# Performance work log

Measured on AMD Instinct MI355X. Metric: run time of the kernel, lower is better.

## Reference

```python
import jax, jax.numpy as jnp
import numpy as np

# Model dims (see init_kwargs)
B, N, N_IN, D = 16, 8192, 4096, 8
DT = 1e-3
TAU_MEM, TAU_ADAPT = 0.02, 0.2
ALPHA = float(np.exp(-DT / TAU_MEM))    # membrane leak decay per step
RHO_A = float(np.exp(-DT / TAU_ADAPT))  # threshold-adaptation decay per step
BETA = 1.8                              # adaptive-threshold strength (ALIF)
TH0 = 1.0                               # base firing threshold
P_SPIKE = 0.05                          # presynaptic firing prob for inputs


def setup_inputs() -> dict:
    key = jax.random.key(0)
    k = jax.random.split(key, 6)
    V = jax.random.normal(k[0], (B, N), jnp.float32)          # membrane potentials
    a = jax.random.uniform(k[1], (B, N), dtype=jnp.float32)   # ALIF adaptation state
    # Delayed-spike ring buffer [D, B, N] and external spikes [B, N_IN] (binary)
    Xd = (jax.random.uniform(k[2], (D, B, N)) < P_SPIKE).astype(jnp.float32)
    Xext = (jax.random.uniform(k[3], (B, N_IN)) < P_SPIKE).astype(jnp.float32)
    # Delta-synapse weights (internal recurrent + one external area)
    W_int = jax.random.normal(k[4], (N, N), jnp.float32) / np.sqrt(N)
    W_ext = jax.random.normal(k[5], (N_IN, N), jnp.float32) / np.sqrt(N_IN)
    return dict(V=V, a=a, Xd=Xd, Xext=Xext, W_int=W_int, W_ext=W_ext)


def reference(V, a, Xd, Xext, W_int, W_ext):
    # --- ALIFSpikes: adaptive threshold spike generation ---
    th = TH0 + BETA * a
    X = (V >= th).astype(V.dtype)            # [B, N] output spikes
    a_new = RHO_A * a + X                    # adaptation integrates spikes
    # --- DeltaSynapse aggregation: internal (delayed) + external currents ---
    current = Xd[-1] @ W_int + Xext @ W_ext  # [B, N]
    # --- Membrane: leaky integrate with reset-on-spike ---
    V_new = ALPHA * V * (1.0 - X) + (1.0 - ALPHA) * current
    # Shift delay buffer (newest spikes enter slot 0)
    Xd_new = jnp.concatenate([X[None], Xd[:-1]], axis=0)
    return X, V_new, a_new, Xd_new
```

## Files before the change

kernel.cpp:

```cpp
#include <hip/hip_runtime.h>
#include <cstdint>
#include <cstddef>

#define NN    8192
#define NIN   4096
#define BB    16
#define BN    131072
#define ITILE 128
#define CINT  64
#define CEXT  32
#define CTOT  96

static constexpr float ALPHA_F = 0.9512294245007140f;
static constexpr float RHOA_F  = 0.9950124791926823f;
static constexpr float SCALE_F = (float)(1.0 - 0.9512294245007140);

__global__ __launch_bounds__(256) void k_prep(
    const float* __restrict__ V, const float* __restrict__ a,
    const float* __restrict__ Xd, const float* __restrict__ Xext,
    float* __restrict__ out,
    unsigned* __restrict__ mask_int, unsigned* __restrict__ mask_ext)
{
    const int t = blockIdx.x * 256 + threadIdx.x;
    const float v  = V[t];
    const float av = a[t];
    const float th = __fadd_rn(1.0f, __fmul_rn(1.8f, av));
    const bool  spike = (v >= th);
    const float x = spike ? 1.0f : 0.0f;
    out[t]          = x;
    out[BN + t]     = spike ? 0.0f : __fmul_rn(ALPHA_F, v);
    out[2*BN + t]   = __fadd_rn(__fmul_rn(RHOA_F, av), x);
    out[3*BN + t]   = x;

    if (t < NN) {
        unsigned m = 0;
        #pragma unroll
        for (int b = 0; b < BB; ++b)
            m |= (Xd[7*BN + b*NN + t] > 0.5f) ? (1u << b) : 0u;
        mask_int[t] = m;
    } else if (t < NN + NIN) {
        const int i = t - NN;
        unsigned m = 0;
        #pragma unroll
        for (int b = 0; b < BB; ++b)
            m |= (Xext[b*NIN + i] > 0.5f) ? (1u << b) : 0u;
        mask_ext[i] = m;
    }
}

__global__ __launch_bounds__(256) void k_shift(const float4* __restrict__ src,
                                               float4* __restrict__ dst)
{
    const int t = blockIdx.x * 256 + threadIdx.x;
    dst[t] = src[t];
}

__device__ __forceinline__ void accrow(float2 (&acc)[BB], unsigned m, float wx, float wy)
{
    #pragma unroll
    for (int b = 0; b < BB; ++b) {
        const float f = (float)((m >> b) & 1u);
        acc[b].x = __builtin_fmaf(wx, f, acc[b].x);
        acc[b].y = __builtin_fmaf(wy, f, acc[b].y);
    }
}

__global__ __launch_bounds__(256) void k_mm(
    const float* __restrict__ Wint, const float* __restrict__ Wext,
    const unsigned* __restrict__ mask_int, const unsigned* __restrict__ mask_ext,
    float* __restrict__ dst, int atomic_mode)
{
    const int tid   = threadIdx.x;
    const int chunk = blockIdx.y;
    const bool is_int = (chunk < CINT);
    const float*    W    = is_int ? Wint : Wext;
    const unsigned* mask = is_int ? mask_int : mask_ext;
    const int i0 = (is_int ? chunk : (chunk - CINT)) * ITILE;

    __shared__ unsigned sm[ITILE];
    if (tid < ITILE) sm[tid] = mask[i0 + tid];
    __syncthreads();

    const int n = (blockIdx.x << 9) + (tid << 1);
    float2 acc[BB];
    #pragma unroll
    for (int b = 0; b < BB; ++b) acc[b] = make_float2(0.f, 0.f);

    const float* Wp = W + (size_t)i0 * NN + n;
    float2 w0 = make_float2(0.f,0.f), w1 = w0, w2 = w0, w3 = w0;

    for (int ii = 0; ii < ITILE; ii += 4) {
        const unsigned m0 = (unsigned)__builtin_amdgcn_readfirstlane((int)sm[ii+0]);
        const unsigned m1 = (unsigned)__builtin_amdgcn_readfirstlane((int)sm[ii+1]);
        const unsigned m2 = (unsigned)__builtin_amdgcn_readfirstlane((int)sm[ii+2]);
        const unsigned m3 = (unsigned)__builtin_amdgcn_readfirstlane((int)sm[ii+3]);
        if (m0) w0 = *(const float2*)(Wp + 0*(size_t)NN);
        if (m1) w1 = *(const float2*)(Wp + 1*(size_t)NN);
        if (m2) w2 = *(const float2*)(Wp + 2*(size_t)NN);
        if (m3) w3 = *(const float2*)(Wp + 3*(size_t)NN);
        if (m0) accrow(acc, m0, w0.x, w0.y);
        if (m1) accrow(acc, m1, w1.x, w1.y);
        if (m2) accrow(acc, m2, w2.x, w2.y);
        if (m3) accrow(acc, m3, w3.x, w3.y);
        Wp += 4*(size_t)NN;
    }

    if (atomic_mode) {
        float* o = dst + n;
        #pragma unroll
        for (int b = 0; b < BB; ++b) {
            unsafeAtomicAdd(o + (size_t)b*NN + 0, SCALE_F * acc[b].x);
            unsafeAtomicAdd(o + (size_t)b*NN + 1, SCALE_F * acc[b].y);
        }
    } else {
        float* p = dst + (size_t)chunk * BN + n;
        #pragma unroll
        for (int b = 0; b < BB; ++b)
            *(float2*)(p + (size_t)b*NN) = acc[b];
    }
}

__global__ __launch_bounds__(256) void k_fin(float* __restrict__ outV,
                                             const float* __restrict__ part)
{
    const int t4 = blockIdx.x * 256 + threadIdx.x;
    float4 s = make_float4(0.f, 0.f, 0.f, 0.f);
    #pragma unroll 8
    for (int c = 0; c < CTOT; ++c) {
        const float4 p = ((const float4*)(part + (size_t)c * BN))[t4];
        s.x += p.x; s.y += p.y; s.z += p.z; s.w += p.w;
    }
    float4 v = ((float4*)outV)[t4];
    v.x = __builtin_fmaf(SCALE_F, s.x, v.x);
    v.y = __builtin_fmaf(SCALE_F, s.y, v.y);
    v.z = __builtin_fmaf(SCALE_F, s.z, v.z);
    v.w = __builtin_fmaf(SCALE_F, s.w, v.w);
    ((float4*)outV)[t4] = v;
}

extern "C" void kernel_launch(void* const* d_in, const int* in_sizes, int n_in,
                              void* d_out, int out_size, void* d_ws, size_t ws_size,
                              hipStream_t stream)
{
    const float* V    = (const float*)d_in[0];
    const float* a    = (const float*)d_in[1];
    const float* Xd   = (const float*)d_in[2];
    const float* Xext = (const float*)d_in[3];
    const float* Wint = (const float*)d_in[4];
    const float* Wext = (const float*)d_in[5];
    float* out = (float*)d_out;

    unsigned* mask_int = (unsigned*)d_ws;
    unsigned* mask_ext = mask_int + NN;
    float*    part     = (float*)((char*)d_ws + 65536);
    const size_t need  = 65536 + (size_t)CTOT * BN * sizeof(float);
    const int atomic_mode = (ws_size < need) ? 1 : 0;

    k_prep<<<BN/256, 256, 0, stream>>>(V, a, Xd, Xext, out, mask_int, mask_ext);
    k_shift<<<(7*BN/4)/256, 256, 0, stream>>>((const float4*)Xd,
                                              (float4*)(out + (size_t)4*BN));
    float* mmdst = atomic_mode ? (out + BN) : part;
    k_mm<<<dim3(16, CTOT), 256, 0, stream>>>(Wint, Wext, mask_int, mask_ext,
                                             mmdst, atomic_mode);
    if (!atomic_mode)
        k_fin<<<BN/4/256, 256, 0, stream>>>(out + BN, part);
}
```

Baseline: 440.6 us.

## Compact active presynaptic rows into lists and load-balance the sparse matmul

Adds a single-block kernel that uses wave ballots to compact nonzero spike-mask rows into packed (row, mask) lists with counts. The matmul then walks only active rows, split evenly across 32 chunks instead of 96 fixed 128-row tiles. This aims to remove per-row branch checks, balance work across blocks, and cut partial-sum write and reduce traffic threefold. In exchange it adds a serial compaction launch and lowers grid size. It also drops the atomic fallback for small workspaces.

```diff
diff --git a/kernel.cpp b/kernel.cpp
--- a/kernel.cpp
+++ b/kernel.cpp
@@ -6,10 +6,9 @@
 #define NIN   4096
 #define BB    16
 #define BN    131072
-#define ITILE 128
-#define CINT  64
-#define CEXT  32
-#define CTOT  96
+#define NCH   32
+#define NCHI  21
+#define NCHE  11
 
 static constexpr float ALPHA_F = 0.9512294245007140f;
 static constexpr float RHOA_F  = 0.9950124791926823f;
@@ -48,6 +47,59 @@
     }
 }
 
+__global__ __launch_bounds__(1024) void k_compact(
+    const unsigned* __restrict__ mask_int, const unsigned* __restrict__ mask_ext,
+    unsigned* __restrict__ cnt,
+    unsigned* __restrict__ list_int, unsigned* __restrict__ list_ext)
+{
+    __shared__ unsigned wsum[16];
+    __shared__ unsigned stot;
+    const int t = threadIdx.x;
+    const int wave = t >> 6, lane = t & 63;
+
+    unsigned base = 0;
+    #pragma unroll 1
+    for (int r = 0; r < 8; ++r) {
+        const int row = r * 1024 + t;
+        const unsigned m = mask_int[row];
+        const unsigned long long bal = __ballot(m != 0);
+        const unsigned pre = __popcll(bal & ((1ull << lane) - 1ull));
+        if (lane == 0) wsum[wave] = (unsigned)__popcll(bal);
+        __syncthreads();
+        if (t == 0) {
+            unsigned s = 0;
+            for (int i = 0; i < 16; ++i) { unsigned c = wsum[i]; wsum[i] = s; s += c; }
+            stot = s;
+        }
+        __syncthreads();
+        if (m) list_int[base + wsum[wave] + pre] = ((unsigned)row << 16) | m;
+        base += stot;
+        __syncthreads();
+    }
+    if (t == 0) cnt[0] = base;
+
+    base = 0;
+    #pragma unroll 1
+    for (int r = 0; r < 4; ++r) {
+        const int row = r * 1024 + t;
+        const unsigned m = mask_ext[row];
+        const unsigned long long bal = __ballot(m != 0);
+        const unsigned pre = __popcll(bal & ((1ull << lane) - 1ull));
+        if (lane == 0) wsum[wave] = (unsigned)__popcll(bal);
+        __syncthreads();
+        if (t == 0) {
+            unsigned s = 0;
+            for (int i = 0; i < 16; ++i) { unsigned c = wsum[i]; wsum[i] = s; s += c; }
+            stot = s;
+        }
+        __syncthreads();
+        if (m) list_ext[base + wsum[wave] + pre] = ((unsigned)row << 16) | m;
+        base += stot;
+        __syncthreads();
+    }
+    if (t == 0) cnt[1] = base;
+}
+
 __global__ __launch_bounds__(256) void k_shift(const float4* __restrict__ src,
                                                float4* __restrict__ dst)
 {
@@ -67,57 +119,54 @@
 
 __global__ __launch_bounds__(256) void k_mm(
     const float* __restrict__ Wint, const float* __restrict__ Wext,
-    const unsigned* __restrict__ mask_int, const unsigned* __restrict__ mask_ext,
-    float* __restrict__ dst, int atomic_mode)
-{
-    const int tid   = threadIdx.x;
-    const int chunk = blockIdx.y;
-    const bool is_int = (chunk < CINT);
+    const unsigned* __restrict__ cnt,
+    const unsigned* __restrict__ list_int, const unsigned* __restrict__ list_ext,
+    float* __restrict__ part)
+{
+    const int tid = threadIdx.x;
+    const int y   = blockIdx.y;
+    const bool is_int = (y < NCHI);
     const float*    W    = is_int ? Wint : Wext;
-    const unsigned* mask = is_int ? mask_int : mask_ext;
-    const int i0 = (is_int ? chunk : (chunk - CINT)) * ITILE;
-
-    __shared__ unsigned sm[ITILE];
-    if (tid < ITILE) sm[tid] = mask[i0 + tid];
-    __syncthreads();
+    const unsigned* list = is_int ? list_int : list_ext;
+    const unsigned  np_  = is_int ? NCHI : NCHE;
+    const unsigned  pi   = is_int ? (unsigned)y : (unsigned)(y - NCHI);
+    const unsigned  c    = cnt[is_int ? 0 : 1];
+    const unsigned  lo   = (pi * c) / np_;
+    const unsigned  hi   = ((pi + 1) * c) / np_;
 
     const int n = (blockIdx.x << 9) + (tid << 1);
+
     float2 acc[BB];
     #pragma unroll
     for (int b = 0; b < BB; ++b) acc[b] = make_float2(0.f, 0.f);
 
-    const float* Wp = W + (size_t)i0 * NN + n;
-    float2 w0 = make_float2(0.f,0.f), w1 = w0, w2 = w0, w3 = w0;
-
-    for (int ii = 0; ii < ITILE; ii += 4) {
-        const unsigned m0 = (unsigned)__builtin_amdgcn_readfirstlane((int)sm[ii+0]);
-        const unsigned m1 = (unsigned)__builtin_amdgcn_readfirstlane((int)sm[ii+1]);
-        const unsigned m2 = (unsigned)__builtin_amdgcn_readfirstlane((int)sm[ii+2]);
-        const unsigned m3 = (unsigned)__builtin_amdgcn_readfirstlane((int)sm[ii+3]);
-        if (m0) w0 = *(const float2*)(Wp + 0*(size_t)NN);
-        if (m1) w1 = *(const float2*)(Wp + 1*(size_t)NN);
-        if (m2) w2 = *(const float2*)(Wp + 2*(size_t)NN);
-        if (m3) w3 = *(const float2*)(Wp + 3*(size_t)NN);
-        if (m0) accrow(acc, m0, w0.x, w0.y);
-        if (m1) accrow(acc, m1, w1.x, w1.y);
-        if (m2) accrow(acc, m2, w2.x, w2.y);
-        if (m3) accrow(acc, m3, w3.x, w3.y);
-        Wp += 4*(size_t)NN;
-    }
-
-    if (atomic_mode) {
-        float* o = dst + n;
-        #pragma unroll
-        for (int b = 0; b < BB; ++b) {
-            unsafeAtomicAdd(o + (size_t)b*NN + 0, SCALE_F * acc[b].x);
-            unsafeAtomicAdd(o + (size_t)b*NN + 1, SCALE_F * acc[b].y);
+    __shared__ unsigned sm[256];
+
+    for (unsigned base = lo; base < hi; base += 256) {
+        const unsigned idx = base + tid;
+        sm[tid] = (idx < hi) ? list[idx] : 0u;
+        __syncthreads();
+        const unsigned tile  = min(256u, hi - base);
+        const unsigned tile8 = (tile + 7u) & ~7u;
+        for (unsigned j = 0; j < tile8; j += 8) {
+            unsigned e[8];
+            float2   w[8];
+            #pragma unroll
+            for (int k = 0; k < 8; ++k) e[k] = sm[j + k];
+            #pragma unroll
+            for (int k = 0; k < 8; ++k)
+                w[k] = *(const float2*)(W + (size_t)(e[k] >> 16) * NN + n);
+            #pragma unroll
+            for (int k = 0; k < 8; ++k)
+                accrow(acc, e[k] & 0xffffu, w[k].x, w[k].y);
         }
-    } else {
-        float* p = dst + (size_t)chunk * BN + n;
-        #pragma unroll
-        for (int b = 0; b < BB; ++b)
-            *(float2*)(p + (size_t)b*NN) = acc[b];
-    }
+        __syncthreads();
+    }
+
+    float* p = part + (size_t)y * BN + n;
+    #pragma unroll
+    for (int b = 0; b < BB; ++b)
+        *(float2*)(p + (size_t)b * NN) = acc[b];
 }
 
 __global__ __launch_bounds__(256) void k_fin(float* __restrict__ outV,
@@ -126,7 +175,7 @@
     const int t4 = blockIdx.x * 256 + threadIdx.x;
     float4 s = make_float4(0.f, 0.f, 0.f, 0.f);
     #pragma unroll 8
-    for (int c = 0; c < CTOT; ++c) {
+    for (int c = 0; c < NCH; ++c) {
         const float4 p = ((const float4*)(part + (size_t)c * BN))[t4];
         s.x += p.x; s.y += p.y; s.z += p.z; s.w += p.w;
     }
@@ -150,18 +199,17 @@
     const float* Wext = (const float*)d_in[5];
     float* out = (float*)d_out;
 
-    unsigned* mask_int = (unsigned*)d_ws;
+    unsigned* cnt      = (unsigned*)d_ws;
+    unsigned* mask_int = (unsigned*)((char*)d_ws + 256);
     unsigned* mask_ext = mask_int + NN;
-    float*    part     = (float*)((char*)d_ws + 65536);
-    const size_t need  = 65536 + (size_t)CTOT * BN * sizeof(float);
-    const int atomic_mode = (ws_size < need) ? 1 : 0;
+    unsigned* list_int = mask_ext + NIN;
+    unsigned* list_ext = list_int + NN;
+    float*    part     = (float*)((char*)d_ws + 131072);
 
     k_prep<<<BN/256, 256, 0, stream>>>(V, a, Xd, Xext, out, mask_int, mask_ext);
+    k_compact<<<1, 1024, 0, stream>>>(mask_int, mask_ext, cnt, list_int, list_ext);
     k_shift<<<(7*BN/4)/256, 256, 0, stream>>>((const float4*)Xd,
                                               (float4*)(out + (size_t)4*BN));
-    float* mmdst = atomic_mode ? (out + BN) : part;
-    k_mm<<<dim3(16, CTOT), 256, 0, stream>>>(Wint, Wext, mask_int, mask_ext,
-                                             mmdst, atomic_mode);
-    if (!atomic_mode)
-        k_fin<<<BN/4/256, 256, 0, stream>>>(out + BN, part);
-}
+    k_mm<<<dim3(16, NCH), 256, 0, stream>>>(Wint, Wext, cnt, list_int, list_ext, part);
+    k_fin<<<BN/4/256, 256, 0, stream>>>(out + BN, part);
+}
```

After: 429.3 us. -2.6%, faster.

## Compact nonzero spike rows per chunk, enlarge row chunks, fuse ALIF into finalize

Applied to the files above, without the earlier changes.

The matmul kernel now builds a compacted list of weight rows that have any active batch spike in each 512-row chunk, using ballot and prefix popcount. It then gathers only those rows, eight at a time, so loads are batched and there is no per-row branch. Chunks grow from 128 to 512 rows, cutting the partial-sum buffer from 96 slices to 24, which shrinks the finalize reduction traffic at the cost of fewer blocks in the matmul grid. The ALIF spike/state update moves into the finalize kernel and the delay-buffer shift merges into the mask kernel, reducing launches. The atomic fallback for small workspace is removed.

```diff
diff --git a/kernel.cpp b/kernel.cpp
--- a/kernel.cpp
+++ b/kernel.cpp
@@ -6,31 +6,21 @@
 #define NIN   4096
 #define BB    16
 #define BN    131072
-#define ITILE 128
-#define CINT  64
-#define CEXT  32
-#define CTOT  96
+#define ROWCH 512
+#define NCHI  16
+#define NCHE  8
+#define NCH   24
 
 static constexpr float ALPHA_F = 0.9512294245007140f;
 static constexpr float RHOA_F  = 0.9950124791926823f;
 static constexpr float SCALE_F = (float)(1.0 - 0.9512294245007140);
 
-__global__ __launch_bounds__(256) void k_prep(
-    const float* __restrict__ V, const float* __restrict__ a,
+__global__ __launch_bounds__(256) void k_aux(
     const float* __restrict__ Xd, const float* __restrict__ Xext,
     float* __restrict__ out,
     unsigned* __restrict__ mask_int, unsigned* __restrict__ mask_ext)
 {
     const int t = blockIdx.x * 256 + threadIdx.x;
-    const float v  = V[t];
-    const float av = a[t];
-    const float th = __fadd_rn(1.0f, __fmul_rn(1.8f, av));
-    const bool  spike = (v >= th);
-    const float x = spike ? 1.0f : 0.0f;
-    out[t]          = x;
-    out[BN + t]     = spike ? 0.0f : __fmul_rn(ALPHA_F, v);
-    out[2*BN + t]   = __fadd_rn(__fmul_rn(RHOA_F, av), x);
-    out[3*BN + t]   = x;
 
     if (t < NN) {
         unsigned m = 0;
@@ -46,13 +36,8 @@
             m |= (Xext[b*NIN + i] > 0.5f) ? (1u << b) : 0u;
         mask_ext[i] = m;
     }
-}
 
-__global__ __launch_bounds__(256) void k_shift(const float4* __restrict__ src,
-                                               float4* __restrict__ dst)
-{
-    const int t = blockIdx.x * 256 + threadIdx.x;
-    dst[t] = src[t];
+    ((float4*)(out + (size_t)4*BN))[t] = ((const float4*)Xd)[t];
 }
 
 __device__ __forceinline__ void accrow(float2 (&acc)[BB], unsigned m, float wx, float wy)
@@ -68,74 +53,101 @@
 __global__ __launch_bounds__(256) void k_mm(
     const float* __restrict__ Wint, const float* __restrict__ Wext,
     const unsigned* __restrict__ mask_int, const unsigned* __restrict__ mask_ext,
-    float* __restrict__ dst, int atomic_mode)
+    float* __restrict__ part)
 {
-    const int tid   = threadIdx.x;
-    const int chunk = blockIdx.y;
-    const bool is_int = (chunk < CINT);
+    const int tid  = threadIdx.x;
+    const int y    = blockIdx.y;
+    const int wave = tid >> 6, lane = tid & 63;
+    const bool is_int = (y < NCHI);
     const float*    W    = is_int ? Wint : Wext;
     const unsigned* mask = is_int ? mask_int : mask_ext;
-    const int i0 = (is_int ? chunk : (chunk - CINT)) * ITILE;
+    const int base_row   = (is_int ? y : (y - NCHI)) * ROWCH;
 
-    __shared__ unsigned sm[ITILE];
-    if (tid < ITILE) sm[tid] = mask[i0 + tid];
+    __shared__ unsigned sc[ROWCH + 8];
+    __shared__ unsigned wsum[4];
+
+    unsigned total = 0;
+    #pragma unroll
+    for (int r = 0; r < 2; ++r) {
+        const int idx = r * 256 + tid;
+        const unsigned m = mask[base_row + idx];
+        const unsigned long long bal = __ballot(m != 0);
+        const unsigned pre = __popcll(bal & ((1ull << lane) - 1ull));
+        if (lane == 0) wsum[wave] = (unsigned)__popcll(bal);
+        __syncthreads();
+        const unsigned w0 = wsum[0], w1 = wsum[1], w2 = wsum[2], w3 = wsum[3];
+        unsigned bw = 0;
+        if (wave > 0) bw += w0;
+        if (wave > 1) bw += w1;
+        if (wave > 2) bw += w2;
+        if (m) sc[total + bw + pre] = ((unsigned)idx << 16) | m;
+        total += w0 + w1 + w2 + w3;
+        __syncthreads();
+    }
+    if (tid < 8) sc[total + tid] = 0u;
     __syncthreads();
+    const unsigned nrow8 = (total + 7u) & ~7u;
 
     const int n = (blockIdx.x << 9) + (tid << 1);
     float2 acc[BB];
     #pragma unroll
     for (int b = 0; b < BB; ++b) acc[b] = make_float2(0.f, 0.f);
 
-    const float* Wp = W + (size_t)i0 * NN + n;
-    float2 w0 = make_float2(0.f,0.f), w1 = w0, w2 = w0, w3 = w0;
-
-    for (int ii = 0; ii < ITILE; ii += 4) {
-        const unsigned m0 = (unsigned)__builtin_amdgcn_readfirstlane((int)sm[ii+0]);
-        const unsigned m1 = (unsigned)__builtin_amdgcn_readfirstlane((int)sm[ii+1]);
-        const unsigned m2 = (unsigned)__builtin_amdgcn_readfirstlane((int)sm[ii+2]);
-        const unsigned m3 = (unsigned)__builtin_amdgcn_readfirstlane((int)sm[ii+3]);
-        if (m0) w0 = *(const float2*)(Wp + 0*(size_t)NN);
-        if (m1) w1 = *(const float2*)(Wp + 1*(size_t)NN);
-        if (m2) w2 = *(const float2*)(Wp + 2*(size_t)NN);
-        if (m3) w3 = *(const float2*)(Wp + 3*(size_t)NN);
-        if (m0) accrow(acc, m0, w0.x, w0.y);
-        if (m1) accrow(acc, m1, w1.x, w1.y);
-        if (m2) accrow(acc, m2, w2.x, w2.y);
-        if (m3) accrow(acc, m3, w3.x, w3.y);
-        Wp += 4*(size_t)NN;
+    const float* Wb = W + (size_t)base_row * NN + n;
+    for (unsigned j = 0; j < nrow8; j += 8) {
+        unsigned e[8];
+        float2   w[8];
+        #pragma unroll
+        for (int k = 0; k < 8; ++k) e[k] = sc[j + k];
+        #pragma unroll
+        for (int k = 0; k < 8; ++k)
+            w[k] = *(const float2*)(Wb + (size_t)(e[k] >> 16) * NN);
+        #pragma unroll
+        for (int k = 0; k < 8; ++k)
+            accrow(acc, e[k] & 0xffffu, w[k].x, w[k].y);
     }
 
-    if (atomic_mode) {
-        float* o = dst + n;
-        #pragma unroll
-        for (int b = 0; b < BB; ++b) {
-            unsafeAtomicAdd(o + (size_t)b*NN + 0, SCALE_F * acc[b].x);
-            unsafeAtomicAdd(o + (size_t)b*NN + 1, SCALE_F * acc[b].y);
-        }
-    } else {
-        float* p = dst + (size_t)chunk * BN + n;
-        #pragma unroll
-        for (int b = 0; b < BB; ++b)
-            *(float2*)(p + (size_t)b*NN) = acc[b];
-    }
+    float* p = part + (size_t)y * BN + n;
+    #pragma unroll
+    for (int b = 0; b < BB; ++b)
+        *(float2*)(p + (size_t)b * NN) = acc[b];
 }
 
-__global__ __launch_bounds__(256) void k_fin(float* __restrict__ outV,
-                                             const float* __restrict__ part)
+__global__ __launch_bounds__(256) void k_fin(
+    const float* __restrict__ V, const float* __restrict__ a,
+    const float* __restrict__ part, float* __restrict__ out)
 {
     const int t4 = blockIdx.x * 256 + threadIdx.x;
+
     float4 s = make_float4(0.f, 0.f, 0.f, 0.f);
     #pragma unroll 8
-    for (int c = 0; c < CTOT; ++c) {
+    for (int c = 0; c < NCH; ++c) {
         const float4 p = ((const float4*)(part + (size_t)c * BN))[t4];
         s.x += p.x; s.y += p.y; s.z += p.z; s.w += p.w;
     }
-    float4 v = ((float4*)outV)[t4];
-    v.x = __builtin_fmaf(SCALE_F, s.x, v.x);
-    v.y = __builtin_fmaf(SCALE_F, s.y, v.y);
-    v.z = __builtin_fmaf(SCALE_F, s.z, v.z);
-    v.w = __builtin_fmaf(SCALE_F, s.w, v.w);
-    ((float4*)outV)[t4] = v;
+
+    const float4 v4 = ((const float4*)V)[t4];
+    const float4 a4 = ((const float4*)a)[t4];
+    float4 x4, vn4, an4;
+    {
+        const float* vv = &v4.x; const float* aa = &a4.x;
+        float* xx = &x4.x; float* vn = &vn4.x; float* an = &an4.x;
+        const float* ss = &s.x;
+        #pragma unroll
+        for (int k = 0; k < 4; ++k) {
+            const float th = __fadd_rn(1.0f, __fmul_rn(1.8f, aa[k]));
+            const bool spike = (vv[k] >= th);
+            const float x = spike ? 1.0f : 0.0f;
+            xx[k] = x;
+            float v_new = spike ? 0.0f : __fmul_rn(ALPHA_F, vv[k]);
+            vn[k] = __builtin_fmaf(SCALE_F, ss[k], v_new);
+            an[k] = __fadd_rn(__fmul_rn(RHOA_F, aa[k]), x);
+        }
+    }
+    ((float4*)out)[t4]                       = x4;
+    ((float4*)(out + (size_t)BN))[t4]        = vn4;
+    ((float4*)(out + (size_t)2*BN))[t4]      = an4;
+    ((float4*)(out + (size_t)3*BN))[t4]      = x4;
 }
 
 extern "C" void kernel_launch(void* const* d_in, const int* in_sizes, int n_in,
@@ -153,15 +165,8 @@
     unsigned* mask_int = (unsigned*)d_ws;
     unsigned* mask_ext = mask_int + NN;
     float*    part     = (float*)((char*)d_ws + 65536);
-    const size_t need  = 65536 + (size_t)CTOT * BN * sizeof(float);
-    const int atomic_mode = (ws_size < need) ? 1 : 0;
 
-    k_prep<<<BN/256, 256, 0, stream>>>(V, a, Xd, Xext, out, mask_int, mask_ext);
-    k_shift<<<(7*BN/4)/256, 256, 0, stream>>>((const float4*)Xd,
-                                              (float4*)(out + (size_t)4*BN));
-    float* mmdst = atomic_mode ? (out + BN) : part;
-    k_mm<<<dim3(16, CTOT), 256, 0, stream>>>(Wint, Wext, mask_int, mask_ext,
-                                             mmdst, atomic_mode);
-    if (!atomic_mode)
-        k_fin<<<BN/4/256, 256, 0, stream>>>(out + BN, part);
+    k_aux<<<(7*BN/4)/256, 256, 0, stream>>>(Xd, Xext, out, mask_int, mask_ext);
+    k_mm<<<dim3(16, NCH), 256, 0, stream>>>(Wint, Wext, mask_int, mask_ext, part);
+    k_fin<<<BN/4/256, 256, 0, stream>>>(V, a, part, out);
 }
```

After: 426.5 us. -3.2%, faster.
